# Performance work log

Hardware: AMD Instinct MI355X
Metric: run time of the kernel (lower is better)

Reference implementation:

```python
import jax, jax.numpy as jnp
import numpy as np

B, N, D, H = 128, 2048, 512, 512

def setup_inputs() -> dict:
    key = jax.random.key(0)
    ks = jax.random.split(key, 8)
    x = jax.random.normal(ks[0], (B, D), dtype=jnp.float32)
    context = jax.random.normal(ks[1], (B, N, D), dtype=jnp.float32)
    mask = jax.random.randint(ks[2], (B, 1, N), 0, 2) > 0  # True = masked out
    Wi = jax.random.normal(ks[3], (H, D), dtype=jnp.float32) * 0.02
    bi = jnp.zeros((H,), dtype=jnp.float32)
    Wc = jax.random.normal(ks[4], (H, D), dtype=jnp.float32) * 0.02
    bc = jnp.zeros((H,), dtype=jnp.float32)
    V = jax.random.uniform(ks[5], (H,), dtype=jnp.float32, minval=-1.0, maxval=1.0)
    return {"x": x, "context": context, "mask": mask,
            "Wi": Wi, "bi": bi, "Wc": Wc, "bc": bc, "V": V}

def reference(x, context, mask, Wi, bi, Wc, bc, V):
    # input_linear: [B, H]
    inp = x @ Wi.T + bi
    # context_linear (Conv1d kernel=1 == pointwise linear): [B, N, H]
    ctx = jnp.einsum('bnd,hd->bnh', context, Wc) + bc
    # additive (Bahdanau) score: V . tanh(inp + ctx) -> [B, N]
    att = jnp.einsum('h,bnh->bn', V, jnp.tanh(inp[:, None, :] + ctx))
    att = jnp.where(mask[:, 0, :], -jnp.inf, att)
    alpha = jax.nn.softmax(att, axis=-1)
    log_p = jax.nn.log_softmax(att, axis=-1)
    # context mixing: bmm(ctx^T [B,H,N], alpha [B,N,1]) -> [B, H]
    hidden_state = jnp.einsum('bnh,bn->bh', ctx, alpha)
    return hidden_state, alpha, log_p
```

## Files before the change

### kernel.cpp

```cpp
#include <hip/hip_runtime.h>
#include <hip/hip_bf16.h>
#include <math.h>

#define B_ 128
#define N_ 2048
#define D_ 512
#define H_ 512

#define NEG_BIG (-1.0e30f)

typedef unsigned int uint;
typedef unsigned short ushort;

#define WS_INP  0
#define WS_ATT  (WS_INP + B_*H_)
#define WS_M    (WS_ATT + B_*N_)
#define WS_FLAG (WS_M + B_*D_)
#define WS_BP   393280
#define WS_NEED_FLOATS (WS_BP + 262144)

typedef __attribute__((ext_vector_type(4))) float  f32x4;
typedef __attribute__((ext_vector_type(8))) short  bf16x8;

union BF8 { unsigned short u[8]; bf16x8 v; };

__device__ __forceinline__ ushort f2bf(float x) {
    uint u = __float_as_uint(x);
    u = (u + 0x7fffu + ((u >> 16) & 1u)) >> 16;
    return (ushort)u;
}
__device__ __forceinline__ float bf2f(ushort h) {
    return __uint_as_float(((uint)h) << 16);
}
__device__ __forceinline__ float fast_tanh(float x) {
    return 1.0f - 2.0f / (1.0f + __expf(2.0f * x));
}

__global__ void detect_mask(const uint* __restrict__ mask_raw,
                            int* __restrict__ flag) {
    int lane = threadIdx.x;
    uint v = mask_raw[lane];
    unsigned long long m = __ballot(v <= 1u);
    if (lane == 0) *flag = (m == ~0ull) ? 1 : 0;
}

__global__ __launch_bounds__(256) void linear_kernel(
        const float* __restrict__ a, const float* __restrict__ W,
        const float* __restrict__ bias, float* __restrict__ out) {
    int idx = blockIdx.x * 256 + threadIdx.x;
    int b = idx >> 9;
    int h = idx & (H_ - 1);
    const float4* ar = (const float4*)(a + (size_t)b * D_);
    const float4* wr = (const float4*)(W + (size_t)h * D_);
    float acc = 0.f;
#pragma unroll 4
    for (int d = 0; d < D_ / 4; ++d) {
        float4 av = ar[d], wv = wr[d];
        acc = fmaf(av.x, wv.x, acc);
        acc = fmaf(av.y, wv.y, acc);
        acc = fmaf(av.z, wv.z, acc);
        acc = fmaf(av.w, wv.w, acc);
    }
    out[idx] = acc + bias[h];
}

__global__ __launch_bounds__(256) void pack_wc(const float* __restrict__ Wc,
                                               ushort* __restrict__ Bp) {
    int tid = blockIdx.x * 256 + threadIdx.x;
    int lane = tid & 63;
    int fs   = tid >> 6;
    int hf = fs >> 4, ks = fs & 15;
    int h  = hf * 16 + (lane & 15);
    int k0 = ks * 32 + (lane >> 4) * 8;
    const float* src = Wc + (size_t)h * D_ + k0;
    BF8 hi, lo;
#pragma unroll
    for (int j = 0; j < 8; ++j) {
        float x = src[j];
        hi.u[j] = f2bf(x);
        lo.u[j] = f2bf(x - bf2f(hi.u[j]));
    }
    *(bf16x8*)(Bp + (size_t)tid * 8)          = hi.v;
    *(bf16x8*)(Bp + 262144 + (size_t)tid * 8) = lo.v;
}

#define KP  32
#define NPH 16

#define DMA_B(p, bi) do {                                                       \
    _Pragma("unroll")                                                           \
    for (int i_ = 0; i_ < 8; ++i_) {                                            \
        int c_  = w * 8 + i_;                                                   \
        int hf_ = c_ & 31;                                                      \
        const ushort* g_ = Bp + (c_ >= 32 ? 262144 : 0)                         \
                         + (size_t)((hf_ << 4) + (p)) * 512 + lane * 8;         \
        ushort* l_ = (c_ >= 32 ? sBl[bi] : sBh[bi]) + hf_ * 512;                \
        __builtin_amdgcn_global_load_lds(                                       \
            (const __attribute__((address_space(1))) unsigned int*)g_,          \
            (__attribute__((address_space(3))) unsigned int*)l_, 16, 0, 0);     \
    }                                                                           \
} while (0)

#define STAGE_A2(Ux, Wx, bi) do {                                               \
    uint h0_ = (Ux.y & 0xFFFF0000u) | (Ux.x >> 16);                             \
    uint h1_ = (Ux.w & 0xFFFF0000u) | (Ux.z >> 16);                             \
    uint h2_ = (Wx.y & 0xFFFF0000u) | (Wx.x >> 16);                             \
    uint h3_ = (Wx.w & 0xFFFF0000u) | (Wx.z >> 16);                             \
    float r0_ = __uint_as_float(Ux.x) - __uint_as_float(Ux.x & 0xFFFF0000u);    \
    float r1_ = __uint_as_float(Ux.y) - __uint_as_float(Ux.y & 0xFFFF0000u);    \
    float r2_ = __uint_as_float(Ux.z) - __uint_as_float(Ux.z & 0xFFFF0000u);    \
    float r3_ = __uint_as_float(Ux.w) - __uint_as_float(Ux.w & 0xFFFF0000u);    \
    float r4_ = __uint_as_float(Wx.x) - __uint_as_float(Wx.x & 0xFFFF0000u);    \
    float r5_ = __uint_as_float(Wx.y) - __uint_as_float(Wx.y & 0xFFFF0000u);    \
    float r6_ = __uint_as_float(Wx.z) - __uint_as_float(Wx.z & 0xFFFF0000u);    \
    float r7_ = __uint_as_float(Wx.w) - __uint_as_float(Wx.w & 0xFFFF0000u);    \
    uint l0_ = (__float_as_uint(r1_) & 0xFFFF0000u) | (__float_as_uint(r0_) >> 16); \
    uint l1_ = (__float_as_uint(r3_) & 0xFFFF0000u) | (__float_as_uint(r2_) >> 16); \
    uint l2_ = (__float_as_uint(r5_) & 0xFFFF0000u) | (__float_as_uint(r4_) >> 16); \
    uint l3_ = (__float_as_uint(r7_) & 0xFFFF0000u) | (__float_as_uint(r6_) >> 16); \
    *(uint4*)((char*)sAh[bi] + aw) = make_uint4(h0_, h1_, h2_, h3_);            \
    *(uint4*)((char*)sAl[bi] + aw) = make_uint4(l0_, l1_, l2_, l3_);            \
} while (0)

#define MM(a_, b_, c_) __builtin_amdgcn_mfma_f32_16x16x32_bf16(a_, b_, c_, 0, 0, 0)

#define CL1(c_, BH, BL) do {                                                    \
    acc[0][c_] = MM(ah0, BH, acc[0][c_]); acc[1][c_] = MM(ah1, BH, acc[1][c_]); \
    acc[2][c_] = MM(ah2, BH, acc[2][c_]); acc[3][c_] = MM(ah3, BH, acc[3][c_]); \
    acc[0][c_] = MM(ah0, BL, acc[0][c_]); acc[1][c_] = MM(ah1, BL, acc[1][c_]); \
    acc[2][c_] = MM(ah2, BL, acc[2][c_]); acc[3][c_] = MM(ah3, BL, acc[3][c_]); \
    acc[0][c_] = MM(al0, BH, acc[0][c_]); acc[1][c_] = MM(al1, BH, acc[1][c_]); \
    acc[2][c_] = MM(al2, BH, acc[2][c_]); acc[3][c_] = MM(al3, BH, acc[3][c_]); \
} while (0)

#define LOADB(cf_, BH, BL) do {                                                 \
    const int bo_ = (wc * 8 + (cf_)) * 512 + lane * 8;                          \
    BH = *(const bf16x8*)&sBh[buf][bo_];                                        \
    BL = *(const bf16x8*)&sBl[buf][bo_];                                        \
} while (0)

#define SB0 __builtin_amdgcn_sched_barrier(0)

__global__ __launch_bounds__(512, 2) void att_mfma_kernel(
        const float* __restrict__ ctx, const ushort* __restrict__ Bp,
        const float* __restrict__ bc, const float* __restrict__ V,
        const float* __restrict__ inp, float* __restrict__ att) {
    __shared__ ushort sAh[2][4096];
    __shared__ ushort sAl[2][4096];
    __shared__ ushort sBh[2][16384];
    __shared__ ushort sBl[2][16384];

    const int t    = threadIdx.x;
    const int lane = t & 63;
    const int w    = t >> 6;
    const int wr   = w >> 2;
    const int wc   = w & 3;
    const int g0   = blockIdx.x * 128;
    const int b    = g0 >> 11;

    const int srow = t >> 2;
    const int skc  = t & 3;
    const float* gAs = ctx + (size_t)(g0 + srow) * D_ + skc * 8;
    unsigned aw = ((unsigned)(srow >> 4) << 10) | ((unsigned)skc << 8)
                | ((unsigned)(srow & 15) << 4);
    aw ^= ((aw >> 8) & 3u) << 4;

    unsigned ar_[4];
#pragma unroll
    for (int rf = 0; rf < 4; ++rf) {
        unsigned o = ((unsigned)(wr * 4 + rf) << 10) | ((unsigned)lane << 4);
        o ^= ((o >> 8) & 3u) << 4;
        ar_[rf] = o;
    }

    f32x4 acc[4][8] = {};

    {
        uint4 U0 = *(const uint4*)(gAs);
        uint4 W0 = *(const uint4*)(gAs + 4);
        SB0;
        DMA_B(0, 0);
        SB0;
        STAGE_A2(U0, W0, 0);
        asm volatile("s_waitcnt lgkmcnt(0)" ::: "memory");
        __builtin_amdgcn_s_barrier();
    }

    for (int p = 0; p < NPH; ++p) {
        const int buf = p & 1;
        const int pn  = (p + 1) & 15;

        uint4 U  = *(const uint4*)(gAs + pn * KP);
        uint4 Wv = *(const uint4*)(gAs + pn * KP + 4);
        SB0;
        DMA_B(pn, buf ^ 1);
        SB0;
        asm volatile("s_waitcnt vmcnt(10)" ::: "memory");
        SB0;

        bf16x8 ah0, al0, ah1, al1, ah2, al2, ah3, al3;
        ah0 = *(const bf16x8*)((const char*)sAh[buf] + ar_[0]);
        al0 = *(const bf16x8*)((const char*)sAl[buf] + ar_[0]);
        ah1 = *(const bf16x8*)((const char*)sAh[buf] + ar_[1]);
        al1 = *(const bf16x8*)((const char*)sAl[buf] + ar_[1]);
        ah2 = *(const bf16x8*)((const char*)sAh[buf] + ar_[2]);
        al2 = *(const bf16x8*)((const char*)sAl[buf] + ar_[2]);
        ah3 = *(const bf16x8*)((const char*)sAh[buf] + ar_[3]);
        al3 = *(const bf16x8*)((const char*)sAl[buf] + ar_[3]);
        bf16x8 bh0, bl0, bh1, bl1;
        LOADB(0, bh0, bl0); LOADB(1, bh1, bl1);
        SB0;
        bf16x8 bh2, bl2, bh3, bl3;
        LOADB(2, bh2, bl2); LOADB(3, bh3, bl3);
        SB0;
        __builtin_amdgcn_s_setprio(1);
        CL1(0, bh0, bl0); CL1(1, bh1, bl1);
        SB0;
        bf16x8 bh4, bl4, bh5, bl5;
        LOADB(4, bh4, bl4); LOADB(5, bh5, bl5);
        SB0;
        CL1(2, bh2, bl2); CL1(3, bh3, bl3);
        SB0;
        bf16x8 bh6, bl6, bh7, bl7;
        LOADB(6, bh6, bl6); LOADB(7, bh7, bl7);
        SB0;
        CL1(4, bh4, bl4); CL1(5, bh5, bl5);
        SB0;
        CL1(6, bh6, bl6); CL1(7, bh7, bl7);
        __builtin_amdgcn_s_setprio(0);
        SB0;

        STAGE_A2(U, Wv, buf ^ 1);
        asm volatile("s_waitcnt lgkmcnt(0)" ::: "memory");
        __builtin_amdgcn_s_barrier();
    }

    float P[4][4] = {};
#pragma unroll
    for (int cf = 0; cf < 8; ++cf) {
        const int h = wc * 128 + cf * 16 + (lane & 15);
        const float sh = inp[b * H_ + h] + bc[h];
        const float vh = V[h];
#pragma unroll
        for (int rf = 0; rf < 4; ++rf)
#pragma unroll
            for (int j = 0; j < 4; ++j)
                P[rf][j] += vh * fast_tanh(acc[rf][cf][j] + sh);
    }
#pragma unroll
    for (int rf = 0; rf < 4; ++rf)
#pragma unroll
        for (int j = 0; j < 4; ++j) {
            float x = P[rf][j];
            x += __shfl_xor(x, 1); x += __shfl_xor(x, 2);
            x += __shfl_xor(x, 4); x += __shfl_xor(x, 8);
            P[rf][j] = x;
        }

    float (*red)[64] = (float(*)[64])sAh;
    if ((lane & 15) == 0) {
        const int kc = lane >> 4;
#pragma unroll
        for (int rf = 0; rf < 4; ++rf)
#pragma unroll
            for (int j = 0; j < 4; ++j)
                red[w][rf * 16 + kc * 4 + j] = P[rf][j];
    }
    __syncthreads();
    if (t < 128) {
        const int wrr = (t >> 6) * 4, r = t & 63;
        att[g0 + t] = red[wrr + 0][r] + red[wrr + 1][r] + red[wrr + 2][r] + red[wrr + 3][r];
    }
}

__global__ __launch_bounds__(256) void softmax_kernel(
        const float* __restrict__ att, const void* __restrict__ mask,
        const int* __restrict__ flag, float* __restrict__ alpha,
        float* __restrict__ logp) {
    __shared__ float row[N_];
    __shared__ float red[4];
    const int b = blockIdx.x, t = threadIdx.x;
    const int is_int = *flag;
    const int* mi = (const int*)mask;
    const unsigned char* mb = (const unsigned char*)mask;

    float lmax = -INFINITY;
    for (int n = t; n < N_; n += 256) {
        bool m = is_int ? (mi[b * N_ + n] != 0) : (mb[b * N_ + n] != 0);
        float a = m ? NEG_BIG : att[b * N_ + n];
        row[n] = a;
        lmax = fmaxf(lmax, a);
    }
#pragma unroll
    for (int off = 32; off; off >>= 1) lmax = fmaxf(lmax, __shfl_down(lmax, off));
    if ((t & 63) == 0) red[t >> 6] = lmax;
    __syncthreads();
    const float rmax = fmaxf(fmaxf(red[0], red[1]), fmaxf(red[2], red[3]));
    __syncthreads();

    float lsum = 0.f;
    for (int n = t; n < N_; n += 256) lsum += __expf(row[n] - rmax);
#pragma unroll
    for (int off = 32; off; off >>= 1) lsum += __shfl_down(lsum, off);
    if ((t & 63) == 0) red[t >> 6] = lsum;
    __syncthreads();
    const float s = red[0] + red[1] + red[2] + red[3];
    const float inv = 1.0f / s;
    const float lse = logf(s);

    for (int n = t; n < N_; n += 256) {
        float a = row[n];
        alpha[b * N_ + n] = __expf(a - rmax) * inv;
        logp[b * N_ + n]  = a - rmax - lse;
    }
}

__global__ __launch_bounds__(512) void wsum_kernel(
        const float* __restrict__ context, const float* __restrict__ alpha,
        float* __restrict__ m) {
    __shared__ float al[N_];
    __shared__ float part[3][128];
    const int c = blockIdx.x;
    const int b = blockIdx.y;
    const int t = threadIdx.x;
    for (int n = t; n < N_; n += 512) al[n] = alpha[(size_t)b * N_ + n];
    __syncthreads();
    const int d = c * 128 + (t & 127);
    const int q = t >> 7;
    const float* cp = context + (size_t)b * N_ * D_ + (size_t)q * 512 * D_ + d;
    const float* ap = al + q * 512;
    float acc = 0.f;
#pragma unroll 8
    for (int n = 0; n < 512; ++n) acc = fmaf(ap[n], cp[(size_t)n * D_], acc);
    if (q) part[q - 1][t & 127] = acc;
    __syncthreads();
    if (q == 0)
        m[b * D_ + d] = acc + part[0][t & 127] + part[1][t & 127] + part[2][t & 127];
}

extern "C" void kernel_launch(void* const* d_in, const int* in_sizes, int n_in,
                              void* d_out, int out_size, void* d_ws, size_t ws_size,
                              hipStream_t stream) {
    const float* x       = (const float*)d_in[0];
    const float* context = (const float*)d_in[1];
    const void*  mask    = d_in[2];
    const float* Wi      = (const float*)d_in[3];
    const float* bi      = (const float*)d_in[4];
    const float* Wc      = (const float*)d_in[5];
    const float* bc      = (const float*)d_in[6];
    const float* V       = (const float*)d_in[7];

    float* out  = (float*)d_out;
    float* ws   = (float*)d_ws;
    float* inp  = ws + WS_INP;
    float* att  = ws + WS_ATT;
    float* m    = ws + WS_M;
    int*   flag = (int*)(ws + WS_FLAG);

    float* hidden = out;
    float* alpha  = out + B_ * H_;
    float* logp   = alpha + B_ * N_;

    ushort* Bp =
        (ws_size >= (size_t)WS_NEED_FLOATS * 4) ? (ushort*)(ws + WS_BP)
                                                : (ushort*)logp;

    detect_mask<<<1, 64, 0, stream>>>((const uint*)mask, flag);
    linear_kernel<<<256, 256, 0, stream>>>(x, Wi, bi, inp);
    pack_wc<<<128, 256, 0, stream>>>(Wc, Bp);
    att_mfma_kernel<<<(B_ * N_) / 128, 512, 0, stream>>>(context, Bp, bc, V, inp, att);
    softmax_kernel<<<B_, 256, 0, stream>>>(att, mask, flag, alpha, logp);
    wsum_kernel<<<dim3(4, B_), 512, 0, stream>>>(context, alpha, m);
    linear_kernel<<<256, 256, 0, stream>>>(m, Wc, bc, hidden);
}
```

Measured before the change: 561.6 us.

## Load B fragments directly from global memory instead of staging through LDS

```diff
diff --git a/kernel.cpp b/kernel.cpp
--- a/kernel.cpp
+++ b/kernel.cpp
@@ -86,20 +86,6 @@
 
 #define KP  32
 #define NPH 16
-
-#define DMA_B(p, bi) do {                                                       \
-    _Pragma("unroll")                                                           \
-    for (int i_ = 0; i_ < 8; ++i_) {                                            \
-        int c_  = w * 8 + i_;                                                   \
-        int hf_ = c_ & 31;                                                      \
-        const ushort* g_ = Bp + (c_ >= 32 ? 262144 : 0)                         \
-                         + (size_t)((hf_ << 4) + (p)) * 512 + lane * 8;         \
-        ushort* l_ = (c_ >= 32 ? sBl[bi] : sBh[bi]) + hf_ * 512;                \
-        __builtin_amdgcn_global_load_lds(                                       \
-            (const __attribute__((address_space(1))) unsigned int*)g_,          \
-            (__attribute__((address_space(3))) unsigned int*)l_, 16, 0, 0);     \
-    }                                                                           \
-} while (0)
 
 #define STAGE_A2(Ux, Wx, bi) do {                                               \
     uint h0_ = (Ux.y & 0xFFFF0000u) | (Ux.x >> 16);                             \
@@ -124,19 +110,24 @@
 
 #define MM(a_, b_, c_) __builtin_amdgcn_mfma_f32_16x16x32_bf16(a_, b_, c_, 0, 0, 0)
 
-#define CL1(c_, BH, BL) do {                                                    \
-    acc[0][c_] = MM(ah0, BH, acc[0][c_]); acc[1][c_] = MM(ah1, BH, acc[1][c_]); \
-    acc[2][c_] = MM(ah2, BH, acc[2][c_]); acc[3][c_] = MM(ah3, BH, acc[3][c_]); \
-    acc[0][c_] = MM(ah0, BL, acc[0][c_]); acc[1][c_] = MM(ah1, BL, acc[1][c_]); \
-    acc[2][c_] = MM(ah2, BL, acc[2][c_]); acc[3][c_] = MM(ah3, BL, acc[3][c_]); \
-    acc[0][c_] = MM(al0, BH, acc[0][c_]); acc[1][c_] = MM(al1, BH, acc[1][c_]); \
-    acc[2][c_] = MM(al2, BH, acc[2][c_]); acc[3][c_] = MM(al3, BH, acc[3][c_]); \
+#define LOADB_G(cf_, BH, BL) do {                                               \
+    BH = *(const bf16x8*)(Bpp + bb + (cf_) * 8192);                             \
+    BL = *(const bf16x8*)(Bpp + 262144 + bb + (cf_) * 8192);                    \
 } while (0)
 
-#define LOADB(cf_, BH, BL) do {                                                 \
-    const int bo_ = (wc * 8 + (cf_)) * 512 + lane * 8;                          \
-    BH = *(const bf16x8*)&sBh[buf][bo_];                                        \
-    BL = *(const bf16x8*)&sBl[buf][bo_];                                        \
+#define MFMA_CF(cf_, BH, BL) do {                                               \
+    acc[0][cf_] = MM(ah[0], BH, acc[0][cf_]);                                   \
+    acc[1][cf_] = MM(ah[1], BH, acc[1][cf_]);                                   \
+    acc[2][cf_] = MM(ah[2], BH, acc[2][cf_]);                                   \
+    acc[3][cf_] = MM(ah[3], BH, acc[3][cf_]);                                   \
+    acc[0][cf_] = MM(ah[0], BL, acc[0][cf_]);                                   \
+    acc[1][cf_] = MM(ah[1], BL, acc[1][cf_]);                                   \
+    acc[2][cf_] = MM(ah[2], BL, acc[2][cf_]);                                   \
+    acc[3][cf_] = MM(ah[3], BL, acc[3][cf_]);                                   \
+    acc[0][cf_] = MM(al[0], BH, acc[0][cf_]);                                   \
+    acc[1][cf_] = MM(al[1], BH, acc[1][cf_]);                                   \
+    acc[2][cf_] = MM(al[2], BH, acc[2][cf_]);                                   \
+    acc[3][cf_] = MM(al[3], BH, acc[3][cf_]);                                   \
 } while (0)
 
 #define SB0 __builtin_amdgcn_sched_barrier(0)
@@ -147,8 +138,6 @@
         const float* __restrict__ inp, float* __restrict__ att) {
     __shared__ ushort sAh[2][4096];
     __shared__ ushort sAl[2][4096];
-    __shared__ ushort sBh[2][16384];
-    __shared__ ushort sBl[2][16384];
 
     const int t    = threadIdx.x;
     const int lane = t & 63;
@@ -173,66 +162,55 @@
         ar_[rf] = o;
     }
 
+    const int bb = wc * 65536 + lane * 8;
+
     f32x4 acc[4][8] = {};
 
     {
         uint4 U0 = *(const uint4*)(gAs);
         uint4 W0 = *(const uint4*)(gAs + 4);
-        SB0;
-        DMA_B(0, 0);
-        SB0;
         STAGE_A2(U0, W0, 0);
-        asm volatile("s_waitcnt lgkmcnt(0)" ::: "memory");
-        __builtin_amdgcn_s_barrier();
+        __syncthreads();
     }
 
     for (int p = 0; p < NPH; ++p) {
         const int buf = p & 1;
         const int pn  = (p + 1) & 15;
+        const ushort* Bpp = Bp + (size_t)p * 512;
 
         uint4 U  = *(const uint4*)(gAs + pn * KP);
         uint4 Wv = *(const uint4*)(gAs + pn * KP + 4);
         SB0;
-        DMA_B(pn, buf ^ 1);
-        SB0;
-        asm volatile("s_waitcnt vmcnt(10)" ::: "memory");
-        SB0;
-
-        bf16x8 ah0, al0, ah1, al1, ah2, al2, ah3, al3;
-        ah0 = *(const bf16x8*)((const char*)sAh[buf] + ar_[0]);
-        al0 = *(const bf16x8*)((const char*)sAl[buf] + ar_[0]);
-        ah1 = *(const bf16x8*)((const char*)sAh[buf] + ar_[1]);
-        al1 = *(const bf16x8*)((const char*)sAl[buf] + ar_[1]);
-        ah2 = *(const bf16x8*)((const char*)sAh[buf] + ar_[2]);
-        al2 = *(const bf16x8*)((const char*)sAl[buf] + ar_[2]);
-        ah3 = *(const bf16x8*)((const char*)sAh[buf] + ar_[3]);
-        al3 = *(const bf16x8*)((const char*)sAl[buf] + ar_[3]);
-        bf16x8 bh0, bl0, bh1, bl1;
-        LOADB(0, bh0, bl0); LOADB(1, bh1, bl1);
-        SB0;
-        bf16x8 bh2, bl2, bh3, bl3;
-        LOADB(2, bh2, bl2); LOADB(3, bh3, bl3);
+        bf16x8 x0h, x0l, x1h, x1l;
+        LOADB_G(0, x0h, x0l); LOADB_G(1, x1h, x1l);
+        SB0;
+        bf16x8 ah[4], al[4];
+#pragma unroll
+        for (int rf = 0; rf < 4; ++rf) {
+            ah[rf] = *(const bf16x8*)((const char*)sAh[buf] + ar_[rf]);
+            al[rf] = *(const bf16x8*)((const char*)sAl[buf] + ar_[rf]);
+        }
+        SB0;
+        bf16x8 y0h, y0l, y1h, y1l;
+        LOADB_G(2, y0h, y0l); LOADB_G(3, y1h, y1l);
         SB0;
         __builtin_amdgcn_s_setprio(1);
-        CL1(0, bh0, bl0); CL1(1, bh1, bl1);
-        SB0;
-        bf16x8 bh4, bl4, bh5, bl5;
-        LOADB(4, bh4, bl4); LOADB(5, bh5, bl5);
-        SB0;
-        CL1(2, bh2, bl2); CL1(3, bh3, bl3);
-        SB0;
-        bf16x8 bh6, bl6, bh7, bl7;
-        LOADB(6, bh6, bl6); LOADB(7, bh7, bl7);
-        SB0;
-        CL1(4, bh4, bl4); CL1(5, bh5, bl5);
-        SB0;
-        CL1(6, bh6, bl6); CL1(7, bh7, bl7);
+        MFMA_CF(0, x0h, x0l); MFMA_CF(1, x1h, x1l);
+        SB0;
+        LOADB_G(4, x0h, x0l); LOADB_G(5, x1h, x1l);
+        SB0;
+        MFMA_CF(2, y0h, y0l); MFMA_CF(3, y1h, y1l);
+        SB0;
+        LOADB_G(6, y0h, y0l); LOADB_G(7, y1h, y1l);
+        SB0;
+        MFMA_CF(4, x0h, x0l); MFMA_CF(5, x1h, x1l);
+        SB0;
+        MFMA_CF(6, y0h, y0l); MFMA_CF(7, y1h, y1l);
         __builtin_amdgcn_s_setprio(0);
         SB0;
 
         STAGE_A2(U, Wv, buf ^ 1);
-        asm volatile("s_waitcnt lgkmcnt(0)" ::: "memory");
-        __builtin_amdgcn_s_barrier();
+        __syncthreads();
     }
 
     float P[4][4] = {};
```

New measurement: 578.3 us. +3.0%, slower.
